# Kernel optimization log

Measured on AMD Instinct MI355X. Metric: run time of the kernel, lower is better.

## Reference

```python
import jax, jax.numpy as jnp
import numpy as np

V = 100000
E = 1600000
IN_CH = 128
HEADS = 4
OUT_CH = 16
NEG_SLOPE = 0.2


def setup_inputs() -> dict:
    key = jax.random.key(0)
    k1, k2, k3, k4, k5 = jax.random.split(key, 5)
    x = jax.random.normal(k1, (V, IN_CH), dtype=jnp.float32)
    edge_index = jax.random.randint(k2, (2, E), 0, V, dtype=jnp.int32)
    # Xavier-ish scaled params
    W = jax.random.normal(k3, (IN_CH, HEADS * OUT_CH), dtype=jnp.float32) / np.sqrt(IN_CH)
    a_src = jax.random.normal(k4, (HEADS, OUT_CH), dtype=jnp.float32) / np.sqrt(OUT_CH)
    a_dst = jax.random.normal(k5, (HEADS, OUT_CH), dtype=jnp.float32) / np.sqrt(OUT_CH)
    return {"x": x, "edge_index": edge_index, "W": W, "a_src": a_src, "a_dst": a_dst}


def reference(x, edge_index, W, a_src, a_dst):
    v = x.shape[0]
    h, cout = a_src.shape
    z = (x @ W).reshape(v, h, cout)                      # [V,H,C]
    src, dst = edge_index[0], edge_index[1]
    # per-node attention logits, then gather at edges (same math as gather-then-dot)
    e_src = jnp.einsum("vhc,hc->vh", z, a_src)           # [V,H]
    e_dst = jnp.einsum("vhc,hc->vh", z, a_dst)           # [V,H]
    e = jax.nn.leaky_relu(e_src[src] + e_dst[dst], NEG_SLOPE)  # [E,H]
    # scatter softmax over dst per head
    m = jax.ops.segment_max(e, dst, num_segments=v)      # [V,H]
    # nodes with no incoming edges get -inf max; edges never reference them
    exp_e = jnp.exp(e - m[dst])                          # [E,H]
    denom = jax.ops.segment_sum(exp_e, dst, num_segments=v)  # [V,H]
    alpha = exp_e / (denom[dst] + 1e-9)                  # [E,H]
    # scatter aggregation of weighted source features
    agg = jax.ops.segment_sum(z[src] * alpha[:, :, None], dst, num_segments=v)  # [V,H,C]
    out = jax.nn.elu(agg)
    return out.reshape(v, h * cout)
```

## Files before the change

### kernel.cpp

```cpp
#include <hip/hip_runtime.h>
#include <hip/hip_bf16.h>
#include <cstdint>

#define NV 100000
#define NE 1600000
#define KIN 128
#define NH 4
#define NC 16
#define NF 64
#define NBKT 391
#define BCAP 4608
#define EPW 16
#define BINWG 391
#define GEMMWG 1563
#define XSTR 136

typedef __attribute__((ext_vector_type(8))) short bf16x8;
typedef __attribute__((ext_vector_type(4))) float f32x4;

__device__ __forceinline__ short f2bf(float f) {
    unsigned u = __float_as_uint(f);
    return (short)((u + 0x7FFFu + ((u >> 16) & 1u)) >> 16);
}

__device__ __forceinline__ unsigned enc11(float w) {
    unsigned t = (__float_as_uint(w) + 0x10000u) >> 17;
    t = min(max(t, 7168u), 9215u);
    return t - 7168u;
}

__global__ __launch_bounds__(256) void k_prep(
    const float* __restrict__ W, short* __restrict__ wfrag,
    int* __restrict__ gcur)
{
    const int t = threadIdx.x;
    for (int i = t; i < NBKT; i += 256) gcur[i] = 0;
#pragma unroll
    for (int it = 0; it < 4; ++it) {
        const int idx = it * 256 + t;
        const int lane = idx & 63;
        const int ctks = idx >> 6;
        const int ct = ctks >> 2, ks = ctks & 3;
        const int n = lane & 15, quad = lane >> 4;
        short* dst = wfrag + (size_t)idx * 8;
#pragma unroll
        for (int j = 0; j < 8; ++j) {
            const int k = ks * 32 + quad * 8 + j;
            dst[j] = f2bf(W[k * NF + ct * 16 + n]);
        }
    }
}

__global__ __launch_bounds__(256) void k_front(
    const float* __restrict__ x, const short* __restrict__ wfrag,
    const float* __restrict__ a_src, const float* __restrict__ a_dst,
    __hip_bfloat16* __restrict__ z, float* __restrict__ esrc,
    float* __restrict__ edst,
    const int* __restrict__ ei, int* __restrict__ gcur,
    unsigned long long* __restrict__ barr)
{
    if (blockIdx.x < BINWG) {
        __shared__ int hist[NBKT];
        __shared__ int base[NBKT];
        const int t = threadIdx.x;
        const int e0 = blockIdx.x * (256 * EPW);
        unsigned* __restrict__ b32 = (unsigned*)barr;

        for (int i = t; i < NBKT; i += 256) hist[i] = 0;
        __syncthreads();

        unsigned pk[EPW];
        short bk[EPW];
#pragma unroll
        for (int i = 0; i < EPW; ++i) {
            const int e = e0 + i * 256 + t;
            if (e < NE) {
                const int s = ei[e];
                const int d = ei[NE + e];
                const int b = d >> 8;
                bk[i] = (short)b;
                pk[i] = ((unsigned)(d & 255) << 17) | (unsigned)s;
                atomicAdd(&hist[b], 1);
            } else {
                bk[i] = -1;
            }
        }
        __syncthreads();
        for (int i = t; i < NBKT; i += 256) {
            const int c = hist[i];
            base[i] = c ? atomicAdd(&gcur[i], c) : 0;
            hist[i] = 0;
        }
        __syncthreads();
#pragma unroll
        for (int i = 0; i < EPW; ++i) {
            if (bk[i] >= 0) {
                const int b = bk[i];
                const int pos = base[b] + atomicAdd(&hist[b], 1);
                b32[(size_t)b * (BCAP * 2) + pos] = pk[i];
            }
        }
    } else {
        __shared__ short xs[64 * XSTR];
        const int t = threadIdx.x;
        const int bb = blockIdx.x - BINWG;
        const float4* __restrict__ x4 = (const float4*)x;

#pragma unroll
        for (int i = 0; i < 8; ++i) {
            const int li = i * 256 + t;
            const int idx = bb * 2048 + li;
            float4 v = make_float4(0.f, 0.f, 0.f, 0.f);
            if (idx < NV * (KIN / 4)) v = x4[idx];
            short* p = &xs[(li >> 5) * XSTR + (li & 31) * 4];
            p[0] = f2bf(v.x); p[1] = f2bf(v.y);
            p[2] = f2bf(v.z); p[3] = f2bf(v.w);
        }
        __syncthreads();

        const int wv = t >> 6;
        const int lane = t & 63;
        const int n = lane & 15;
        const int quad = lane >> 4;

        bf16x8 bf[16];
        const bf16x8* __restrict__ wf = (const bf16x8*)wfrag;
#pragma unroll
        for (int i = 0; i < 16; ++i) bf[i] = wf[i * 64 + lane];

        const short* __restrict__ arow = &xs[(wv * 16 + n) * XSTR];
        f32x4 acc[4];
#pragma unroll
        for (int ct = 0; ct < 4; ++ct) acc[ct] = (f32x4){0.f, 0.f, 0.f, 0.f};

#pragma unroll
        for (int ks = 0; ks < 4; ++ks) {
            const bf16x8 af = *(const bf16x8*)(arow + ks * 32 + quad * 8);
#pragma unroll
            for (int ct = 0; ct < 4; ++ct)
                acc[ct] = __builtin_amdgcn_mfma_f32_16x16x32_bf16(
                    af, bf[ct * 4 + ks], acc[ct], 0, 0, 0);
        }

        float as[4], ad[4];
#pragma unroll
        for (int ct = 0; ct < 4; ++ct) {
            as[ct] = a_src[ct * 16 + n];
            ad[ct] = a_dst[ct * 16 + n];
        }
        unsigned short* __restrict__ zz = (unsigned short*)z;
#pragma unroll
        for (int ct = 0; ct < 4; ++ct) {
#pragma unroll
            for (int reg = 0; reg < 4; ++reg) {
                const int r_g = bb * 64 + wv * 16 + quad * 4 + reg;
                const float v = acc[ct][reg];
                float ps = v * as[ct];
                float pd = v * ad[ct];
#pragma unroll
                for (int m = 8; m >= 1; m >>= 1) {
                    ps += __shfl_xor(ps, m, 16);
                    pd += __shfl_xor(pd, m, 16);
                }
                if (r_g < NV) {
                    zz[(size_t)r_g * NF + ct * 16 + n] = (unsigned short)f2bf(v);
                    if (n == 0) {
                        esrc[r_g * NH + ct] = ps;
                        edst[r_g * NH + ct] = pd;
                    }
                }
            }
        }
    }
}

__global__ __launch_bounds__(512) void k_csr(
    const int* __restrict__ gcur, unsigned long long* __restrict__ barr,
    int* __restrict__ row, int* __restrict__ deg,
    const float* __restrict__ esrc, const float* __restrict__ edst)
{
    __shared__ unsigned arr[BCAP];
    __shared__ int hist[256];
    __shared__ int off[256];
    __shared__ float4 led[256];
    const int t = threadIdx.x;
    const int b = blockIdx.x;
    const int f = gcur[b];
    unsigned* __restrict__ bp32 = (unsigned*)(barr + (size_t)b * BCAP);
    unsigned long long* __restrict__ bp64 = barr + (size_t)b * BCAP;

    for (int i = t; i < f; i += 512) arr[i] = bp32[i];
    if (t < 256) {
        hist[t] = 0;
        const int d = b * 256 + t;
        led[t] = (d < NV) ? *(const float4*)(edst + (size_t)d * 4)
                          : make_float4(0.f, 0.f, 0.f, 0.f);
    }
    __syncthreads();
    for (int i = t; i < f; i += 512) atomicAdd(&hist[arr[i] >> 17], 1);
    __syncthreads();
    if (t < 256) off[t] = hist[t];
    __syncthreads();
    for (int s = 1; s < 256; s <<= 1) {
        const int v = (t < 256 && t >= s) ? off[t - s] : 0;
        __syncthreads();
        if (t < 256) off[t] += v;
        __syncthreads();
    }
    if (t < 256) {
        const int excl = off[t] - hist[t];
        const int d = b * 256 + t;
        if (d < NV) {
            row[d] = b * BCAP + excl;
            deg[d] = hist[t];
        }
        off[t] = excl;
        hist[t] = 0;
    }
    __syncthreads();
    for (int i = t; i < f; i += 512) {
        const unsigned p = arr[i];
        const int dl = p >> 17;
        const unsigned s = p & 0x1FFFFu;
        const int slot = off[dl] + atomicAdd(&hist[dl], 1);
        const float4 e4 = *(const float4*)(esrc + (size_t)s * 4);
        const float4 ed = led[dl];
        float ev;
        ev = e4.x + ed.x; ev = ev > 0.f ? ev : 0.2f * ev;
        const unsigned w0 = enc11(__expf(ev));
        ev = e4.y + ed.y; ev = ev > 0.f ? ev : 0.2f * ev;
        const unsigned w1 = enc11(__expf(ev));
        ev = e4.z + ed.z; ev = ev > 0.f ? ev : 0.2f * ev;
        const unsigned w2 = enc11(__expf(ev));
        ev = e4.w + ed.w; ev = ev > 0.f ? ev : 0.2f * ev;
        const unsigned w3 = enc11(__expf(ev));
        unsigned long long rec = s
            | ((unsigned long long)w0 << 17)
            | ((unsigned long long)w1 << 28)
            | ((unsigned long long)w2 << 39)
            | ((unsigned long long)w3 << 50);
        bp64[slot] = rec;
    }
}

__global__ __launch_bounds__(256) void k_agg(
    const int* __restrict__ row, const int* __restrict__ deg,
    const unsigned long long* __restrict__ recs,
    const __hip_bfloat16* __restrict__ z, float* __restrict__ out)
{
    __shared__ unsigned long long lsw[4][64];
    const int wv = threadIdx.x >> 6;
    const int lane = threadIdx.x & 63;
    const int quad = lane >> 4;
    const int li = lane & 15;
    const int sh = 17 + 11 * (li >> 2);
    const int d = (blockIdx.x * 256 + threadIdx.x) >> 6;
    const int begin = row[d];
    const int nd = deg[d];
    const unsigned short* __restrict__ z16 = (const unsigned short*)z;

    float a0 = 0.f, a1 = 0.f, a2 = 0.f, a3 = 0.f, den = 0.f;
    for (int base = 0; base < nd; base += 64) {
        const int n = min(64, nd - base);
        const unsigned long long rec =
            (lane < n) ? recs[(size_t)begin + base + lane] : 0ull;
        lsw[wv][lane] = rec;
#pragma unroll 4
        for (int j = 0; j < n; j += 4) {
            const unsigned long long r = lsw[wv][j + quad];
            const unsigned s = (unsigned)r & 0x1FFFFu;
            const unsigned wu = ((unsigned)(r >> sh)) & 0x7FFu;
            const float w = __uint_as_float((wu + 7168u) << 17);
            const uint2 zv = *(const uint2*)(z16 + ((size_t)s << 6) + li * 4);
            a0 = fmaf(w, __uint_as_float(zv.x << 16), a0);
            a1 = fmaf(w, __uint_as_float(zv.x & 0xFFFF0000u), a1);
            a2 = fmaf(w, __uint_as_float(zv.y << 16), a2);
            a3 = fmaf(w, __uint_as_float(zv.y & 0xFFFF0000u), a3);
            den += w;
        }
    }
    a0 += __shfl_xor(a0, 16); a0 += __shfl_xor(a0, 32);
    a1 += __shfl_xor(a1, 16); a1 += __shfl_xor(a1, 32);
    a2 += __shfl_xor(a2, 16); a2 += __shfl_xor(a2, 32);
    a3 += __shfl_xor(a3, 16); a3 += __shfl_xor(a3, 32);
    den += __shfl_xor(den, 16); den += __shfl_xor(den, 32);
    if (lane < 16) {
        const float id = 1.f / (den + 1e-9f);
        float v0 = a0 * id, v1 = a1 * id, v2 = a2 * id, v3 = a3 * id;
        v0 = v0 > 0.f ? v0 : __expf(v0) - 1.f;
        v1 = v1 > 0.f ? v1 : __expf(v1) - 1.f;
        v2 = v2 > 0.f ? v2 : __expf(v2) - 1.f;
        v3 = v3 > 0.f ? v3 : __expf(v3) - 1.f;
        *(float4*)(out + (size_t)d * NF + li * 4) = make_float4(v0, v1, v2, v3);
    }
}

extern "C" void kernel_launch(void* const* d_in, const int* in_sizes, int n_in,
                              void* d_out, int out_size, void* d_ws, size_t ws_size,
                              hipStream_t stream)
{
    const float* x     = (const float*)d_in[0];
    const int*   ei    = (const int*)d_in[1];
    const float* W     = (const float*)d_in[2];
    const float* a_src = (const float*)d_in[3];
    const float* a_dst = (const float*)d_in[4];
    float* out = (float*)d_out;

    char* p = (char*)d_ws;
    __hip_bfloat16* z = (__hip_bfloat16*)p;  p += (size_t)NV * NF * 2;
    float* esrc = (float*)p;                 p += (size_t)NV * NH * 4;
    float* edst = (float*)p;                 p += (size_t)NV * NH * 4;
    int*   row  = (int*)p;                   p += (size_t)NV * 4;
    int*   deg  = (int*)p;                   p += (size_t)NV * 4;
    int*   gcur = (int*)p;                   p += (size_t)NBKT * 4;
    p = (char*)(((uintptr_t)p + 255) & ~(uintptr_t)255);
    short* wfrag = (short*)p;                p += (size_t)1024 * 8 * 2;
    p = (char*)(((uintptr_t)p + 255) & ~(uintptr_t)255);
    unsigned long long* barr = (unsigned long long*)p;
    p += (size_t)NBKT * BCAP * 8;

    k_prep<<<1, 256, 0, stream>>>(W, wfrag, gcur);
    k_front<<<BINWG + GEMMWG, 256, 0, stream>>>(x, wfrag, a_src, a_dst, z,
                                                esrc, edst, ei, gcur, barr);
    k_csr<<<NBKT, 512, 0, stream>>>(gcur, barr, row, deg, esrc, edst);
    k_agg<<<(NV * 64) / 256, 256, 0, stream>>>(row, deg, barr, z, out);
}
```

Measured before the change: 188.6 us.

## Fuse CSR build and aggregation into one kernel with LDS-resident edge records

```diff
diff --git a/kernel.cpp b/kernel.cpp
--- a/kernel.cpp
+++ b/kernel.cpp
@@ -8,8 +8,8 @@
 #define NH 4
 #define NC 16
 #define NF 64
-#define NBKT 391
-#define BCAP 4608
+#define NBKT 782
+#define BCAP 2432
 #define EPW 16
 #define BINWG 391
 #define GEMMWG 1563
@@ -57,14 +57,13 @@
     __hip_bfloat16* __restrict__ z, float* __restrict__ esrc,
     float* __restrict__ edst,
     const int* __restrict__ ei, int* __restrict__ gcur,
-    unsigned long long* __restrict__ barr)
+    unsigned* __restrict__ barr)
 {
-    if (blockIdx.x < BINWG) {
+    if (blockIdx.x % 5 == 0) {
         __shared__ int hist[NBKT];
         __shared__ int base[NBKT];
         const int t = threadIdx.x;
-        const int e0 = blockIdx.x * (256 * EPW);
-        unsigned* __restrict__ b32 = (unsigned*)barr;
+        const int e0 = (blockIdx.x / 5) * (256 * EPW);
 
         for (int i = t; i < NBKT; i += 256) hist[i] = 0;
         __syncthreads();
@@ -77,9 +76,9 @@
             if (e < NE) {
                 const int s = ei[e];
                 const int d = ei[NE + e];
-                const int b = d >> 8;
+                const int b = d >> 7;
                 bk[i] = (short)b;
-                pk[i] = ((unsigned)(d & 255) << 17) | (unsigned)s;
+                pk[i] = ((unsigned)(d & 127) << 17) | (unsigned)s;
                 atomicAdd(&hist[b], 1);
             } else {
                 bk[i] = -1;
@@ -97,13 +96,13 @@
             if (bk[i] >= 0) {
                 const int b = bk[i];
                 const int pos = base[b] + atomicAdd(&hist[b], 1);
-                b32[(size_t)b * (BCAP * 2) + pos] = pk[i];
+                barr[(size_t)b * BCAP + pos] = pk[i];
             }
         }
     } else {
         __shared__ short xs[64 * XSTR];
         const int t = threadIdx.x;
-        const int bb = blockIdx.x - BINWG;
+        const int bb = blockIdx.x - blockIdx.x / 5 - 1;
         const float4* __restrict__ x4 = (const float4*)x;
 
 #pragma unroll
@@ -174,55 +173,47 @@
     }
 }
 
-__global__ __launch_bounds__(512) void k_csr(
-    const int* __restrict__ gcur, unsigned long long* __restrict__ barr,
-    int* __restrict__ row, int* __restrict__ deg,
-    const float* __restrict__ esrc, const float* __restrict__ edst)
+__global__ __launch_bounds__(512) void k_back(
+    const int* __restrict__ gcur, const unsigned* __restrict__ barr,
+    const float* __restrict__ esrc, const float* __restrict__ edst,
+    const __hip_bfloat16* __restrict__ z, float* __restrict__ out)
 {
     __shared__ unsigned arr[BCAP];
-    __shared__ int hist[256];
-    __shared__ int off[256];
-    __shared__ float4 led[256];
+    __shared__ unsigned long long rec[BCAP];
+    __shared__ int hist[128], off[128], cur[128];
+    __shared__ float4 led[128];
     const int t = threadIdx.x;
     const int b = blockIdx.x;
     const int f = gcur[b];
-    unsigned* __restrict__ bp32 = (unsigned*)(barr + (size_t)b * BCAP);
-    unsigned long long* __restrict__ bp64 = barr + (size_t)b * BCAP;
-
-    for (int i = t; i < f; i += 512) arr[i] = bp32[i];
-    if (t < 256) {
+    const unsigned* __restrict__ bp = barr + (size_t)b * BCAP;
+
+    for (int i = t; i < f; i += 512) arr[i] = bp[i];
+    if (t < 128) {
         hist[t] = 0;
-        const int d = b * 256 + t;
+        cur[t] = 0;
+        const int d = b * 128 + t;
         led[t] = (d < NV) ? *(const float4*)(edst + (size_t)d * 4)
                           : make_float4(0.f, 0.f, 0.f, 0.f);
     }
     __syncthreads();
     for (int i = t; i < f; i += 512) atomicAdd(&hist[arr[i] >> 17], 1);
     __syncthreads();
-    if (t < 256) off[t] = hist[t];
-    __syncthreads();
-    for (int s = 1; s < 256; s <<= 1) {
-        const int v = (t < 256 && t >= s) ? off[t - s] : 0;
-        __syncthreads();
-        if (t < 256) off[t] += v;
-        __syncthreads();
-    }
-    if (t < 256) {
-        const int excl = off[t] - hist[t];
-        const int d = b * 256 + t;
-        if (d < NV) {
-            row[d] = b * BCAP + excl;
-            deg[d] = hist[t];
-        }
-        off[t] = excl;
-        hist[t] = 0;
-    }
-    __syncthreads();
+    if (t < 128) off[t] = hist[t];
+    __syncthreads();
+    for (int s = 1; s < 128; s <<= 1) {
+        const int v = (t < 128 && t >= s) ? off[t - s] : 0;
+        __syncthreads();
+        if (t < 128) off[t] += v;
+        __syncthreads();
+    }
+    if (t < 128) off[t] -= hist[t];
+    __syncthreads();
+
     for (int i = t; i < f; i += 512) {
         const unsigned p = arr[i];
         const int dl = p >> 17;
         const unsigned s = p & 0x1FFFFu;
-        const int slot = off[dl] + atomicAdd(&hist[dl], 1);
+        const int slot = off[dl] + atomicAdd(&cur[dl], 1);
         const float4 e4 = *(const float4*)(esrc + (size_t)s * 4);
         const float4 ed = led[dl];
         float ev;
@@ -234,40 +225,31 @@
         const unsigned w2 = enc11(__expf(ev));
         ev = e4.w + ed.w; ev = ev > 0.f ? ev : 0.2f * ev;
         const unsigned w3 = enc11(__expf(ev));
-        unsigned long long rec = s
+        rec[slot] = (unsigned long long)s
             | ((unsigned long long)w0 << 17)
             | ((unsigned long long)w1 << 28)
             | ((unsigned long long)w2 << 39)
             | ((unsigned long long)w3 << 50);
-        bp64[slot] = rec;
-    }
-}
-
-__global__ __launch_bounds__(256) void k_agg(
-    const int* __restrict__ row, const int* __restrict__ deg,
-    const unsigned long long* __restrict__ recs,
-    const __hip_bfloat16* __restrict__ z, float* __restrict__ out)
-{
-    __shared__ unsigned long long lsw[4][64];
-    const int wv = threadIdx.x >> 6;
-    const int lane = threadIdx.x & 63;
+    }
+    __syncthreads();
+
+    const int wv = t >> 6;
+    const int lane = t & 63;
     const int quad = lane >> 4;
     const int li = lane & 15;
     const int sh = 17 + 11 * (li >> 2);
-    const int d = (blockIdx.x * 256 + threadIdx.x) >> 6;
-    const int begin = row[d];
-    const int nd = deg[d];
     const unsigned short* __restrict__ z16 = (const unsigned short*)z;
 
-    float a0 = 0.f, a1 = 0.f, a2 = 0.f, a3 = 0.f, den = 0.f;
-    for (int base = 0; base < nd; base += 64) {
-        const int n = min(64, nd - base);
-        const unsigned long long rec =
-            (lane < n) ? recs[(size_t)begin + base + lane] : 0ull;
-        lsw[wv][lane] = rec;
-#pragma unroll 4
-        for (int j = 0; j < n; j += 4) {
-            const unsigned long long r = lsw[wv][j + quad];
+    for (int k = 0; k < 16; ++k) {
+        const int dl = wv + k * 8;
+        const int d = b * 128 + dl;
+        const int begin = off[dl];
+        const int nd = hist[dl];
+        float a0 = 0.f, a1 = 0.f, a2 = 0.f, a3 = 0.f, den = 0.f;
+        for (int j = 0; j < nd; j += 4) {
+            const int je = j + quad;
+            unsigned long long r = 0ull;
+            if (je < nd) r = rec[begin + je];
             const unsigned s = (unsigned)r & 0x1FFFFu;
             const unsigned wu = ((unsigned)(r >> sh)) & 0x7FFu;
             const float w = __uint_as_float((wu + 7168u) << 17);
@@ -278,20 +260,21 @@
             a3 = fmaf(w, __uint_as_float(zv.y & 0xFFFF0000u), a3);
             den += w;
         }
-    }
-    a0 += __shfl_xor(a0, 16); a0 += __shfl_xor(a0, 32);
-    a1 += __shfl_xor(a1, 16); a1 += __shfl_xor(a1, 32);
-    a2 += __shfl_xor(a2, 16); a2 += __shfl_xor(a2, 32);
-    a3 += __shfl_xor(a3, 16); a3 += __shfl_xor(a3, 32);
-    den += __shfl_xor(den, 16); den += __shfl_xor(den, 32);
-    if (lane < 16) {
-        const float id = 1.f / (den + 1e-9f);
-        float v0 = a0 * id, v1 = a1 * id, v2 = a2 * id, v3 = a3 * id;
-        v0 = v0 > 0.f ? v0 : __expf(v0) - 1.f;
-        v1 = v1 > 0.f ? v1 : __expf(v1) - 1.f;
-        v2 = v2 > 0.f ? v2 : __expf(v2) - 1.f;
-        v3 = v3 > 0.f ? v3 : __expf(v3) - 1.f;
-        *(float4*)(out + (size_t)d * NF + li * 4) = make_float4(v0, v1, v2, v3);
+        a0 += __shfl_xor(a0, 16); a0 += __shfl_xor(a0, 32);
+        a1 += __shfl_xor(a1, 16); a1 += __shfl_xor(a1, 32);
+        a2 += __shfl_xor(a2, 16); a2 += __shfl_xor(a2, 32);
+        a3 += __shfl_xor(a3, 16); a3 += __shfl_xor(a3, 32);
+        den += __shfl_xor(den, 16); den += __shfl_xor(den, 32);
+        if (lane < 16 && d < NV) {
+            const float id = 1.f / (den + 1e-9f);
+            float v0 = a0 * id, v1 = a1 * id, v2 = a2 * id, v3 = a3 * id;
+            v0 = v0 > 0.f ? v0 : __expf(v0) - 1.f;
+            v1 = v1 > 0.f ? v1 : __expf(v1) - 1.f;
+            v2 = v2 > 0.f ? v2 : __expf(v2) - 1.f;
+            v3 = v3 > 0.f ? v3 : __expf(v3) - 1.f;
+            *(float4*)(out + (size_t)d * NF + li * 4) =
+                make_float4(v0, v1, v2, v3);
+        }
     }
 }
 
@@ -310,18 +293,14 @@
     __hip_bfloat16* z = (__hip_bfloat16*)p;  p += (size_t)NV * NF * 2;
     float* esrc = (float*)p;                 p += (size_t)NV * NH * 4;
     float* edst = (float*)p;                 p += (size_t)NV * NH * 4;
-    int*   row  = (int*)p;                   p += (size_t)NV * 4;
-    int*   deg  = (int*)p;                   p += (size_t)NV * 4;
     int*   gcur = (int*)p;                   p += (size_t)NBKT * 4;
     p = (char*)(((uintptr_t)p + 255) & ~(uintptr_t)255);
     short* wfrag = (short*)p;                p += (size_t)1024 * 8 * 2;
     p = (char*)(((uintptr_t)p + 255) & ~(uintptr_t)255);
-    unsigned long long* barr = (unsigned long long*)p;
-    p += (size_t)NBKT * BCAP * 8;
+    unsigned* barr = (unsigned*)p;           p += (size_t)NBKT * BCAP * 4;
 
     k_prep<<<1, 256, 0, stream>>>(W, wfrag, gcur);
     k_front<<<BINWG + GEMMWG, 256, 0, stream>>>(x, wfrag, a_src, a_dst, z,
                                                 esrc, edst, ei, gcur, barr);
-    k_csr<<<NBKT, 512, 0, stream>>>(gcur, barr, row, deg, esrc, edst);
-    k_agg<<<(NV * 64) / 256, 256, 0, stream>>>(row, deg, barr, z, out);
-}
+    k_back<<<NBKT, 512, 0, stream>>>(gcur, barr, esrc, edst, z, out);
+}
```

New measurement: 180.7 us. 4.2% less time.
